# Optimization experiments

Measured on AMD Instinct MI355X. Metric: run time of the kernel, lower is better.

The kernel has to match this reference:

```python
import jax, jax.numpy as jnp
import numpy as np

NEG_INF = -1e9
LN_EPS = 1e-5

N, F_IN, F_OUT, H = 4096, 128, 64, 4


def setup_inputs() -> dict:
    key = jax.random.key(0)
    ks = jax.random.split(key, 8)
    return {
        "nodes_features": jax.random.normal(ks[0], (N, F_IN), jnp.float32),
        "degree_matrix": jax.random.normal(ks[1], (N, N), jnp.float32),
        "edges_features_distance": jax.random.normal(ks[2], (N, N), jnp.float32),
        "edges_features_bond": jax.random.normal(ks[3], (N, N), jnp.float32),
        "proj_param": jax.random.normal(ks[4], (H, F_IN, F_OUT), jnp.float32) * 0.1,
        "score_src": jax.random.normal(ks[5], (H, F_OUT, 1), jnp.float32) * 0.1,
        "score_tgt": jax.random.normal(ks[6], (H, F_OUT, 1), jnp.float32) * 0.1,
        "skip_w": jax.random.normal(ks[7], (H * F_OUT, F_IN), jnp.float32) * 0.1,
        "cutoff": 0,
    }


def reference(nodes_features, degree_matrix, edges_features_distance,
              edges_features_bond, proj_param, score_src, score_tgt,
              skip_w, cutoff):
    # connectivity mask: nested where on degree/bond matrices  [N, N]
    wdm = degree_matrix + edges_features_bond
    mask = jnp.where(wdm > 0, wdm,
                     jnp.where(edges_features_bond > cutoff,
                               edges_features_bond + wdm, NEG_INF))

    # per-head projection: [H, N, F_out]
    proj = jnp.einsum('nf,hfo->hno', nodes_features, proj_param)

    # scalar scores per node per head: [H, N, 1]
    s_src = jnp.einsum('hno,hop->hnp', proj, score_src)
    s_tgt = jnp.einsum('hno,hop->hnp', proj, score_tgt)

    # broadcast score matrix [H, N, N]; softmax over dim=1 (as in the original)
    scores = jax.nn.leaky_relu(s_src + jnp.swapaxes(s_tgt, 1, 2), negative_slope=0.2)
    attn = jax.nn.softmax(scores + mask[None, :, :], axis=1)

    # weighted aggregation: [H, N, F_out] -> [N, H, F_out]
    out = jnp.einsum('hij,hjf->hif', attn, proj)
    out = jnp.swapaxes(out, 0, 1)

    # skip connection (F_in != F_out -> linear skip projection)
    skip = (nodes_features @ skip_w.T).reshape(-1, H, F_OUT)
    out = out + skip

    # concat heads, ELU activation (no bias: ctor passes bias=None)
    out = jax.nn.elu(out.reshape(-1, H * F_OUT))

    # fresh LayerNorm (weight=1, bias=0) over last dim of mask
    mu = jnp.mean(mask, axis=-1, keepdims=True)
    var = jnp.var(mask, axis=-1, keepdims=True)
    mask_ln = (mask - mu) / jnp.sqrt(var + LN_EPS)

    return out, mask_ln
```

## Files before the change

### kernel.cpp

```cpp
#include <hip/hip_runtime.h>
#include <math.h>

constexpr int kN  = 4096;
constexpr int kFI = 128;
constexpr int kFO = 64;
constexpr int kH  = 4;
constexpr int kHF = 256;
constexpr float kNegInf = -1e9f;
constexpr float kLnEps  = 1e-5f;

typedef short bf16x8 __attribute__((ext_vector_type(8)));
typedef float f32x4  __attribute__((ext_vector_type(4)));

__device__ __forceinline__ float lrelu(float x){ return x >= 0.f ? x : 0.2f*x; }

__device__ __forceinline__ float wave_sum(float v){
  #pragma unroll
  for (int s = 32; s > 0; s >>= 1) v += __shfl_xor(v, s, 64);
  return v;
}

__device__ __forceinline__ unsigned short f2bf(float x){
  unsigned u = __float_as_uint(x);
  u = (u + 0x7fffu + ((u >> 16) & 1u)) >> 16;
  return (unsigned short)u;
}
__device__ __forceinline__ unsigned f2bf_pk(float a, float b){
  return (unsigned)f2bf(a) | ((unsigned)f2bf(b) << 16);
}

__global__ __launch_bounds__(256) void k_proj(
    const float* __restrict__ nodes, const float* __restrict__ pp,
    const float* __restrict__ ssrc,  const float* __restrict__ stgt,
    const float* __restrict__ skw,
    float* __restrict__ proj, float* __restrict__ ga, float* __restrict__ gb,
    float* __restrict__ skipo)
{
  __shared__ float feat[16][kFI];
  const int tid = threadIdx.x;
  const int n0  = blockIdx.x * 16;
  for (int idx = tid; idx < 16*kFI; idx += 256)
    feat[idx >> 7][idx & 127] = nodes[n0*kFI + idx];
  __syncthreads();
  const int h = tid >> 6, o = tid & 63;
  float accP[16], accS[16];
  #pragma unroll
  for (int n = 0; n < 16; ++n){ accP[n] = 0.f; accS[n] = 0.f; }
  for (int k = 0; k < kFI; ++k){
    const float p = pp[(h*kFI + k)*kFO + o];
    const float w = skw[tid*kFI + k];
    #pragma unroll
    for (int n = 0; n < 16; ++n){
      const float f = feat[n][k];
      accP[n] = fmaf(f, p, accP[n]);
      accS[n] = fmaf(f, w, accS[n]);
    }
  }
  const float sa = ssrc[h*kFO + o];
  const float sb = stgt[h*kFO + o];
  #pragma unroll
  for (int n = 0; n < 16; ++n){
    proj[(h*kN + n0+n)*kFO + o] = accP[n];
    skipo[(n0+n)*kHF + tid]     = accS[n];
    const float va = wave_sum(accP[n] * sa);
    const float vb = wave_sum(accP[n] * sb);
    if (o == 0){ ga[h*kN + n0+n] = va; gb[h*kN + n0+n] = vb; }
  }
}

__global__ __launch_bounds__(256) void k_colsum(
    const float* __restrict__ degm, const float* __restrict__ bondm,
    const float* __restrict__ ga,   const float* __restrict__ gb,
    const int* __restrict__ cutp,
    float* __restrict__ S, float* __restrict__ statg,
    float* __restrict__ maskws, int write_mask)
{
  const int j0 = (blockIdx.x * 256 + threadIdx.x) * 4;
  const int lane = threadIdx.x & 63;
  const float cut = (float)cutp[0];
  float4 bv[kH]; f32x4 sv[kH];
  #pragma unroll
  for (int h = 0; h < kH; ++h){
    bv[h] = *(const float4*)&gb[h*kN + j0];
    sv[h] = (f32x4){0.f, 0.f, 0.f, 0.f};
  }
  const int i0 = blockIdx.y * 32;
  for (int ib = 0; ib < 32; ib += 4){
    float4 dg[4], bd[4];
    #pragma unroll
    for (int u = 0; u < 4; ++u){
      const size_t off = (size_t)(i0+ib+u)*kN + j0;
      dg[u] = *(const float4*)&degm[off];
      bd[u] = *(const float4*)&bondm[off];
    }
    #pragma unroll
    for (int u = 0; u < 4; ++u){
      const int i = i0 + ib + u;
      float4 m;
      {
        float w0 = dg[u].x + bd[u].x, w1 = dg[u].y + bd[u].y;
        float w2 = dg[u].z + bd[u].z, w3 = dg[u].w + bd[u].w;
        m.x = w0 > 0.f ? w0 : (bd[u].x > cut ? bd[u].x + w0 : kNegInf);
        m.y = w1 > 0.f ? w1 : (bd[u].y > cut ? bd[u].y + w1 : kNegInf);
        m.z = w2 > 0.f ? w2 : (bd[u].z > cut ? bd[u].z + w2 : kNegInf);
        m.w = w3 > 0.f ? w3 : (bd[u].w > cut ? bd[u].w + w3 : kNegInf);
      }
      if (write_mask) *(float4*)&maskws[(size_t)i*kN + j0] = m;
      float rsum = (m.x + m.y) + (m.z + m.w);
      float rsq  = fmaf(m.x, m.x, fmaf(m.y, m.y, fmaf(m.z, m.z, m.w*m.w)));
      rsum = wave_sum(rsum); rsq = wave_sum(rsq);
      if (lane == 0){
        atomicAdd(&statg[2*i+0], rsum);
        atomicAdd(&statg[2*i+1], rsq);
      }
      #pragma unroll
      for (int h = 0; h < kH; ++h){
        const float a = ga[h*kN + i];
        sv[h][0] += __expf(lrelu(a + bv[h].x) + m.x);
        sv[h][1] += __expf(lrelu(a + bv[h].y) + m.y);
        sv[h][2] += __expf(lrelu(a + bv[h].z) + m.z);
        sv[h][3] += __expf(lrelu(a + bv[h].w) + m.w);
      }
    }
  }
  #pragma unroll
  for (int h = 0; h < kH; ++h){
    atomicAdd(&S[h*kN + j0+0], sv[h][0]);
    atomicAdd(&S[h*kN + j0+1], sv[h][1]);
    atomicAdd(&S[h*kN + j0+2], sv[h][2]);
    atomicAdd(&S[h*kN + j0+3], sv[h][3]);
  }
}

__global__ __launch_bounds__(256) void k_stat(
    const float* __restrict__ statg, float* __restrict__ statg2)
{
  const int i = blockIdx.x * 256 + threadIdx.x;
  const float mu  = statg[2*i] * (1.f/kN);
  const float var = statg[2*i+1] * (1.f/kN) - mu*mu;
  statg2[2*i+0] = mu;
  statg2[2*i+1] = rsqrtf(var + kLnEps);
}

__global__ __launch_bounds__(256) void k_pack(
    const float* __restrict__ proj, const float* __restrict__ S,
    unsigned short* __restrict__ pSpack)
{
  const int t = blockIdx.x * 256 + threadIdx.x;
  const int L  = t & 63;
  const int nt = (t >> 6) & 3;
  const int kb = (t >> 8) & 127;
  const int h  = t >> 15;
  const int f  = nt*16 + (L & 15);
  const int jb = kb*32 + (L >> 4)*8;
  union { unsigned short s[8]; uint4 v; } u;
  #pragma unroll
  for (int r = 0; r < 8; ++r){
    const int j = jb + r;
    u.s[r] = f2bf(proj[(size_t)(h*kN + j)*kFO + f] / S[h*kN + j]);
  }
  ((uint4*)pSpack)[t] = u.v;
}

__global__ __launch_bounds__(512) void k_aggr(
    const float* __restrict__ degm, const float* __restrict__ bondm,
    const float* __restrict__ maskws, int have_mask,
    const float* __restrict__ ga, const float* __restrict__ gb,
    const int* __restrict__ cutp,
    const unsigned short* __restrict__ pSpack,
    const float* __restrict__ statg2,
    float* __restrict__ accg, float* __restrict__ mlnp)
{
  __shared__ unsigned short ebuf[kH][32][72];
  const int tid = threadIdx.x;
  const int w   = tid >> 6;
  const int L   = tid & 63;
  const int h   = w & 3;
  const int rg  = w >> 2;
  const int r0  = blockIdx.x * 32;
  const int jq0 = blockIdx.y * 1024;
  const float cut = (float)cutp[0];

  const int jp = tid & 31;
  const int ia = tid >> 5;

  float av[2][kH];
  float mu[2], rs[2];
  #pragma unroll
  for (int p = 0; p < 2; ++p){
    const int i = r0 + p*16 + ia;
    #pragma unroll
    for (int hh = 0; hh < kH; ++hh) av[p][hh] = ga[hh*kN + i];
    mu[p] = statg2[2*i+0];
    rs[p] = statg2[2*i+1];
  }

  f32x4 acc[4];
  #pragma unroll
  for (int nt = 0; nt < 4; ++nt) acc[nt] = (f32x4){0.f,0.f,0.f,0.f};

  for (int c = 0; c < 16; ++c){
    const int jb = jq0 + c*64;
    const int jg = jb + 2*jp;
    {
      float2 m2[2];
      if (have_mask){
        #pragma unroll
        for (int p = 0; p < 2; ++p)
          m2[p] = *(const float2*)&maskws[(size_t)(r0 + p*16 + ia)*kN + jg];
      } else {
        #pragma unroll
        for (int p = 0; p < 2; ++p){
          const size_t off = (size_t)(r0 + p*16 + ia)*kN + jg;
          const float2 dg = *(const float2*)&degm[off];
          const float2 bd = *(const float2*)&bondm[off];
          float w0 = dg.x + bd.x, w1 = dg.y + bd.y;
          m2[p].x = w0 > 0.f ? w0 : (bd.x > cut ? bd.x + w0 : kNegInf);
          m2[p].y = w1 > 0.f ? w1 : (bd.y > cut ? bd.y + w1 : kNegInf);
        }
      }
      float2 bv[kH];
      #pragma unroll
      for (int hh = 0; hh < kH; ++hh)
        bv[hh] = *(const float2*)&gb[hh*kN + jg];
      #pragma unroll
      for (int p = 0; p < 2; ++p){
        const int i = p*16 + ia;
        float2 o;
        o.x = (m2[p].x - mu[p]) * rs[p];
        o.y = (m2[p].y - mu[p]) * rs[p];
        *(float2*)&mlnp[(size_t)(r0+i)*kN + jg] = o;
        #pragma unroll
        for (int hh = 0; hh < kH; ++hh){
          const float e0 = __expf(lrelu(av[p][hh] + bv[hh].x) + m2[p].x);
          const float e1 = __expf(lrelu(av[p][hh] + bv[hh].y) + m2[p].y);
          *(unsigned*)&ebuf[hh][i][2*jp] = f2bf_pk(e0, e1);
        }
      }
    }
    __syncthreads();
    {
      const int kb0 = (jb >> 5);
      #pragma unroll
      for (int ks = 0; ks < 2; ++ks){
        const bf16x8 a = *(const bf16x8*)&ebuf[h][rg*16 + (L & 15)][ks*32 + (L >> 4)*8];
        const int kb = kb0 + ks;
        #pragma unroll
        for (int nt = 0; nt < 4; ++nt){
          const bf16x8 b = *(const bf16x8*)&pSpack[(size_t)(((h*128 + kb)*4 + nt)*64 + L)*8];
          acc[nt] = __builtin_amdgcn_mfma_f32_16x16x32_bf16(a, b, acc[nt], 0, 0, 0);
        }
      }
    }
    __syncthreads();
  }

  #pragma unroll
  for (int nt = 0; nt < 4; ++nt){
    #pragma unroll
    for (int reg = 0; reg < 4; ++reg){
      const int i = r0 + rg*16 + (L >> 4)*4 + reg;
      const int f = h*64 + nt*16 + (L & 15);
      atomicAdd(&accg[(size_t)i*kHF + f], acc[nt][reg]);
    }
  }
}

__global__ __launch_bounds__(256) void k_out(
    const float* __restrict__ accg, const float* __restrict__ skipo,
    float* __restrict__ outp)
{
  const int idx = blockIdx.x * 256 + threadIdx.x;
  float o = accg[idx] + skipo[idx];
  o = o > 0.f ? o : expm1f(o);
  outp[idx] = o;
}

extern "C" void kernel_launch(void* const* d_in, const int* in_sizes, int n_in,
                              void* d_out, int out_size, void* d_ws, size_t ws_size,
                              hipStream_t stream)
{
  const float* nodes = (const float*)d_in[0];
  const float* degm  = (const float*)d_in[1];
  const float* bondm = (const float*)d_in[3];
  const float* pp    = (const float*)d_in[4];
  const float* ssrc  = (const float*)d_in[5];
  const float* stgt  = (const float*)d_in[6];
  const float* skw   = (const float*)d_in[7];
  const int*   cutp  = (const int*)d_in[8];

  float* ws    = (float*)d_ws;
  float* proj  = ws;
  float* ga    = proj + (size_t)kH*kN*kFO;
  float* gb    = ga + kH*kN;
  float* S     = gb + kH*kN;
  float* skip  = S + kH*kN;
  float* accg  = skip + (size_t)kN*kHF;
  float* statg = accg + (size_t)kN*kHF;
  float* statg2= statg + 2*kN;
  unsigned short* pSpack = (unsigned short*)(statg2 + 2*kN);
  float* mask  = (float*)(pSpack + (size_t)kH*kN*kFO);

  const size_t base_floats = (size_t)kH*kN*kFO + 3*(size_t)kH*kN
                           + 2*(size_t)kN*kHF + 4*kN
                           + ((size_t)kH*kN*kFO)/2;
  const size_t need_mask = (base_floats + (size_t)kN*kN) * sizeof(float);
  const int have_mask = (ws_size >= need_mask) ? 1 : 0;

  float* outp = (float*)d_out;
  float* mlnp = outp + (size_t)kN*kHF;

  hipMemsetAsync(S, 0, kH*kN*sizeof(float), stream);
  hipMemsetAsync(accg, 0, (size_t)kN*kHF*sizeof(float), stream);
  hipMemsetAsync(statg, 0, 2*kN*sizeof(float), stream);

  k_proj<<<kN/16, 256, 0, stream>>>(nodes, pp, ssrc, stgt, skw, proj, ga, gb, skip);
  k_colsum<<<dim3(kN/1024, kN/32), 256, 0, stream>>>(degm, bondm, ga, gb, cutp,
                                                     S, statg, mask, have_mask);
  k_stat<<<kN/256, 256, 0, stream>>>(statg, statg2);
  k_pack<<<(kH*128*4*64)/256, 256, 0, stream>>>(proj, S, pSpack);
  k_aggr<<<dim3(kN/32, 4), 512, 0, stream>>>(degm, bondm, mask, have_mask,
                                             ga, gb, cutp, pSpack, statg2,
                                             accg, mlnp);
  k_out<<<(kN*kHF)/256, 256, 0, stream>>>(accg, skip, outp);
}
```

Baseline: 365.3 us.

## Shrink aggregation and column-sum tiles, transpose skip weights for coalesced loads

Adds a small kernel that transposes the skip-projection weights so k_proj reads them coalesced across threads instead of strided by 128. The column-sum kernel now covers 8 rows per block instead of 32, launching more blocks. The aggregation kernel is restructured to 16-row tiles with 256 threads and 512-column chunks, where each wave handles one head and each thread processes float4 mask segments. The aim is more blocks and better load width on the memory-bound N×N passes, at the cost of more atomics on the column sums and the output accumulator and re-reading pSpack for each 16-row tile.

```diff
diff --git a/kernel.cpp b/kernel.cpp
--- a/kernel.cpp
+++ b/kernel.cpp
@@ -29,10 +29,18 @@
   return (unsigned)f2bf(a) | ((unsigned)f2bf(b) << 16);
 }
 
+__global__ __launch_bounds__(256) void k_tr(
+    const float* __restrict__ skw, float* __restrict__ skwT)
+{
+  const int k  = blockIdx.x;
+  const int hf = threadIdx.x;
+  skwT[k*kHF + hf] = skw[hf*kFI + k];
+}
+
 __global__ __launch_bounds__(256) void k_proj(
     const float* __restrict__ nodes, const float* __restrict__ pp,
     const float* __restrict__ ssrc,  const float* __restrict__ stgt,
-    const float* __restrict__ skw,
+    const float* __restrict__ skwT,
     float* __restrict__ proj, float* __restrict__ ga, float* __restrict__ gb,
     float* __restrict__ skipo)
 {
@@ -48,7 +56,7 @@
   for (int n = 0; n < 16; ++n){ accP[n] = 0.f; accS[n] = 0.f; }
   for (int k = 0; k < kFI; ++k){
     const float p = pp[(h*kFI + k)*kFO + o];
-    const float w = skw[tid*kFI + k];
+    const float w = skwT[k*kHF + tid];
     #pragma unroll
     for (int n = 0; n < 16; ++n){
       const float f = feat[n][k];
@@ -84,8 +92,8 @@
     bv[h] = *(const float4*)&gb[h*kN + j0];
     sv[h] = (f32x4){0.f, 0.f, 0.f, 0.f};
   }
-  const int i0 = blockIdx.y * 32;
-  for (int ib = 0; ib < 32; ib += 4){
+  const int i0 = blockIdx.y * 8;
+  for (int ib = 0; ib < 8; ib += 4){
     float4 dg[4], bd[4];
     #pragma unroll
     for (int u = 0; u < 4; ++u){
@@ -162,7 +170,7 @@
   ((uint4*)pSpack)[t] = u.v;
 }
 
-__global__ __launch_bounds__(512) void k_aggr(
+__global__ __launch_bounds__(256) void k_aggr(
     const float* __restrict__ degm, const float* __restrict__ bondm,
     const float* __restrict__ maskws, int have_mask,
     const float* __restrict__ ga, const float* __restrict__ gb,
@@ -171,71 +179,59 @@
     const float* __restrict__ statg2,
     float* __restrict__ accg, float* __restrict__ mlnp)
 {
-  __shared__ unsigned short ebuf[kH][32][72];
+  __shared__ unsigned short ebuf[kH][16][72];
   const int tid = threadIdx.x;
   const int w   = tid >> 6;
   const int L   = tid & 63;
-  const int h   = w & 3;
-  const int rg  = w >> 2;
-  const int r0  = blockIdx.x * 32;
-  const int jq0 = blockIdx.y * 1024;
+  const int r0  = blockIdx.x * 16;
+  const int jq0 = blockIdx.y * 512;
+  const int ia  = tid >> 4;
+  const int jq  = tid & 15;
   const float cut = (float)cutp[0];
 
-  const int jp = tid & 31;
-  const int ia = tid >> 5;
-
-  float av[2][kH];
-  float mu[2], rs[2];
-  #pragma unroll
-  for (int p = 0; p < 2; ++p){
-    const int i = r0 + p*16 + ia;
-    #pragma unroll
-    for (int hh = 0; hh < kH; ++hh) av[p][hh] = ga[hh*kN + i];
-    mu[p] = statg2[2*i+0];
-    rs[p] = statg2[2*i+1];
-  }
+  float av[kH];
+  #pragma unroll
+  for (int hh = 0; hh < kH; ++hh) av[hh] = ga[hh*kN + r0 + ia];
+  const float mu = statg2[2*(r0+ia)+0];
+  const float rs = statg2[2*(r0+ia)+1];
 
   f32x4 acc[4];
   #pragma unroll
   for (int nt = 0; nt < 4; ++nt) acc[nt] = (f32x4){0.f,0.f,0.f,0.f};
 
-  for (int c = 0; c < 16; ++c){
+  for (int c = 0; c < 8; ++c){
     const int jb = jq0 + c*64;
-    const int jg = jb + 2*jp;
     {
-      float2 m2[2];
+      const int jg = jb + 4*jq;
+      const size_t off = (size_t)(r0+ia)*kN + jg;
+      float4 m;
       if (have_mask){
-        #pragma unroll
-        for (int p = 0; p < 2; ++p)
-          m2[p] = *(const float2*)&maskws[(size_t)(r0 + p*16 + ia)*kN + jg];
+        m = *(const float4*)&maskws[off];
       } else {
-        #pragma unroll
-        for (int p = 0; p < 2; ++p){
-          const size_t off = (size_t)(r0 + p*16 + ia)*kN + jg;
-          const float2 dg = *(const float2*)&degm[off];
-          const float2 bd = *(const float2*)&bondm[off];
-          float w0 = dg.x + bd.x, w1 = dg.y + bd.y;
-          m2[p].x = w0 > 0.f ? w0 : (bd.x > cut ? bd.x + w0 : kNegInf);
-          m2[p].y = w1 > 0.f ? w1 : (bd.y > cut ? bd.y + w1 : kNegInf);
-        }
-      }
-      float2 bv[kH];
+        const float4 dg = *(const float4*)&degm[off];
+        const float4 bd = *(const float4*)&bondm[off];
+        float w0 = dg.x + bd.x, w1 = dg.y + bd.y;
+        float w2 = dg.z + bd.z, w3 = dg.w + bd.w;
+        m.x = w0 > 0.f ? w0 : (bd.x > cut ? bd.x + w0 : kNegInf);
+        m.y = w1 > 0.f ? w1 : (bd.y > cut ? bd.y + w1 : kNegInf);
+        m.z = w2 > 0.f ? w2 : (bd.z > cut ? bd.z + w2 : kNegInf);
+        m.w = w3 > 0.f ? w3 : (bd.w > cut ? bd.w + w3 : kNegInf);
+      }
+      float4 o;
+      o.x = (m.x - mu) * rs;  o.y = (m.y - mu) * rs;
+      o.z = (m.z - mu) * rs;  o.w = (m.w - mu) * rs;
+      *(float4*)&mlnp[off] = o;
       #pragma unroll
-      for (int hh = 0; hh < kH; ++hh)
-        bv[hh] = *(const float2*)&gb[hh*kN + jg];
-      #pragma unroll
-      for (int p = 0; p < 2; ++p){
-        const int i = p*16 + ia;
-        float2 o;
-        o.x = (m2[p].x - mu[p]) * rs[p];
-        o.y = (m2[p].y - mu[p]) * rs[p];
-        *(float2*)&mlnp[(size_t)(r0+i)*kN + jg] = o;
-        #pragma unroll
-        for (int hh = 0; hh < kH; ++hh){
-          const float e0 = __expf(lrelu(av[p][hh] + bv[hh].x) + m2[p].x);
-          const float e1 = __expf(lrelu(av[p][hh] + bv[hh].y) + m2[p].y);
-          *(unsigned*)&ebuf[hh][i][2*jp] = f2bf_pk(e0, e1);
-        }
+      for (int hh = 0; hh < kH; ++hh){
+        const float4 bv = *(const float4*)&gb[hh*kN + jg];
+        const float e0 = __expf(lrelu(av[hh] + bv.x) + m.x);
+        const float e1 = __expf(lrelu(av[hh] + bv.y) + m.y);
+        const float e2 = __expf(lrelu(av[hh] + bv.z) + m.z);
+        const float e3 = __expf(lrelu(av[hh] + bv.w) + m.w);
+        uint2 u;
+        u.x = f2bf_pk(e0, e1);
+        u.y = f2bf_pk(e2, e3);
+        *(uint2*)&ebuf[hh][ia][4*jq] = u;
       }
     }
     __syncthreads();
@@ -243,11 +239,11 @@
       const int kb0 = (jb >> 5);
       #pragma unroll
       for (int ks = 0; ks < 2; ++ks){
-        const bf16x8 a = *(const bf16x8*)&ebuf[h][rg*16 + (L & 15)][ks*32 + (L >> 4)*8];
+        const bf16x8 a = *(const bf16x8*)&ebuf[w][L & 15][ks*32 + (L >> 4)*8];
         const int kb = kb0 + ks;
         #pragma unroll
         for (int nt = 0; nt < 4; ++nt){
-          const bf16x8 b = *(const bf16x8*)&pSpack[(size_t)(((h*128 + kb)*4 + nt)*64 + L)*8];
+          const bf16x8 b = *(const bf16x8*)&pSpack[(size_t)(((w*128 + kb)*4 + nt)*64 + L)*8];
           acc[nt] = __builtin_amdgcn_mfma_f32_16x16x32_bf16(a, b, acc[nt], 0, 0, 0);
         }
       }
@@ -259,8 +255,8 @@
   for (int nt = 0; nt < 4; ++nt){
     #pragma unroll
     for (int reg = 0; reg < 4; ++reg){
-      const int i = r0 + rg*16 + (L >> 4)*4 + reg;
-      const int f = h*64 + nt*16 + (L & 15);
+      const int i = r0 + (L >> 4)*4 + reg;
+      const int f = w*64 + nt*16 + (L & 15);
       atomicAdd(&accg[(size_t)i*kHF + f], acc[nt][reg]);
     }
   }
@@ -298,11 +294,12 @@
   float* accg  = skip + (size_t)kN*kHF;
   float* statg = accg + (size_t)kN*kHF;
   float* statg2= statg + 2*kN;
-  unsigned short* pSpack = (unsigned short*)(statg2 + 2*kN);
+  float* skwT  = statg2 + 2*kN;
+  unsigned short* pSpack = (unsigned short*)(skwT + (size_t)kFI*kHF);
   float* mask  = (float*)(pSpack + (size_t)kH*kN*kFO);
 
   const size_t base_floats = (size_t)kH*kN*kFO + 3*(size_t)kH*kN
-                           + 2*(size_t)kN*kHF + 4*kN
+                           + 2*(size_t)kN*kHF + 4*kN + (size_t)kFI*kHF
                            + ((size_t)kH*kN*kFO)/2;
   const size_t need_mask = (base_floats + (size_t)kN*kN) * sizeof(float);
   const int have_mask = (ws_size >= need_mask) ? 1 : 0;
@@ -314,12 +311,13 @@
   hipMemsetAsync(accg, 0, (size_t)kN*kHF*sizeof(float), stream);
   hipMemsetAsync(statg, 0, 2*kN*sizeof(float), stream);
 
-  k_proj<<<kN/16, 256, 0, stream>>>(nodes, pp, ssrc, stgt, skw, proj, ga, gb, skip);
-  k_colsum<<<dim3(kN/1024, kN/32), 256, 0, stream>>>(degm, bondm, ga, gb, cutp,
-                                                     S, statg, mask, have_mask);
+  k_tr<<<kFI, 256, 0, stream>>>(skw, skwT);
+  k_proj<<<kN/16, 256, 0, stream>>>(nodes, pp, ssrc, stgt, skwT, proj, ga, gb, skip);
+  k_colsum<<<dim3(kN/1024, kN/8), 256, 0, stream>>>(degm, bondm, ga, gb, cutp,
+                                                    S, statg, mask, have_mask);
   k_stat<<<kN/256, 256, 0, stream>>>(statg, statg2);
   k_pack<<<(kH*128*4*64)/256, 256, 0, stream>>>(proj, S, pSpack);
-  k_aggr<<<dim3(kN/32, 4), 512, 0, stream>>>(degm, bondm, mask, have_mask,
+  k_aggr<<<dim3(kN/16, 8), 256, 0, stream>>>(degm, bondm, mask, have_mask,
                                              ga, gb, cutp, pSpack, statg2,
                                              accg, mlnp);
   k_out<<<(kN*kHF)/256, 256, 0, stream>>>(accg, skip, outp);
```

Result: slower. 456.1 us (+24.8%).
